# Kernel optimization log

Hardware: AMD Instinct MI355X
Metric: run time of the kernel (lower is better)

## Reference

```python
import jax, jax.numpy as jnp
import numpy as np

H, KVH, D, EPS = 8, 4, 64, 1e-5

def _rmsnorm(x, w):
    # normalize over last dim (head_dim)
    norm = jax.lax.rsqrt(jnp.mean(x * x, axis=-1, keepdims=True) + EPS)
    return x * norm * w

def setup_inputs() -> dict:
    key = jax.random.key(0)
    ks = jax.random.split(key, 5)
    B, S, Hid = 2048, 67, 512
    x = jax.random.normal(ks[0], (B, S, Hid), dtype=jnp.float32)
    # weights stored as [in, out] (equivalent to torch Linear weight.T)
    sc = 1.0 / np.sqrt(Hid)
    wq = jax.random.normal(ks[1], (Hid, H * D), dtype=jnp.float32) * sc
    wk = jax.random.normal(ks[2], (Hid, KVH * D), dtype=jnp.float32) * sc
    wv = jax.random.normal(ks[3], (Hid, KVH * D), dtype=jnp.float32) * sc
    wo = jax.random.normal(ks[4], (H * D, Hid), dtype=jnp.float32) * sc
    q_norm_w = jnp.ones((D,), dtype=jnp.float32)
    k_norm_w = jnp.ones((D,), dtype=jnp.float32)
    return {"x": x, "wq": wq, "wk": wk, "wv": wv, "wo": wo,
            "q_norm_w": q_norm_w, "k_norm_w": k_norm_w}

def reference(x, wq, wk, wv, wo, q_norm_w, k_norm_w):
    B, S, _ = x.shape
    G = H // KVH  # query heads per kv head
    q = (x @ wq).reshape(B, S, H, D).transpose(0, 2, 1, 3)      # (B,H,S,D)
    k = (x @ wk).reshape(B, S, KVH, D).transpose(0, 2, 1, 3)    # (B,KVH,S,D)
    v = (x @ wv).reshape(B, S, KVH, D).transpose(0, 2, 1, 3)
    q = _rmsnorm(q, q_norm_w)
    k = _rmsnorm(k, k_norm_w)
    qg = q.reshape(B, KVH, G, S, D)
    scale = 1.0 / np.sqrt(D)
    # bidirectional GQA attention, no mask
    scores = jnp.einsum('bkgsd,bktd->bkgst', qg, k) * scale      # (B,KVH,G,S,S)
    attn = jax.nn.softmax(scores, axis=-1)
    out = jnp.einsum('bkgst,bktd->bkgsd', attn, v)               # (B,KVH,G,S,D)
    out = out.reshape(B, H, S, D).transpose(0, 2, 1, 3).reshape(B, S, H * D)
    return out @ wo
```

## Files before the change

### kernel.cpp

```cpp
#include <hip/hip_runtime.h>
#include <hip/hip_bf16.h>

typedef __attribute__((ext_vector_type(8))) short short8;
typedef __attribute__((ext_vector_type(4))) float f32x4;

#define B_   2048
#define S_   67
#define M_   (B_*S_)
#define HID_ 512
#define H_   8
#define KVH_ 4
#define D_   64

__device__ __forceinline__ unsigned f2bf_u(float f){
  union { __hip_bfloat16 h; unsigned short u; } c; c.h = __float2bfloat16(f); return (unsigned)c.u;
}
__device__ __forceinline__ float bfu2f(unsigned u){
  union { unsigned short u; __hip_bfloat16 h; } c; c.u = (unsigned short)u; return __bfloat162float(c.h);
}
__device__ __forceinline__ unsigned pack2(float a, float b){ return f2bf_u(a) | (f2bf_u(b) << 16); }

__device__ __forceinline__ void unpack8(uint4 v, float* o){
  o[0]=bfu2f(v.x & 0xffffu); o[1]=bfu2f(v.x >> 16);
  o[2]=bfu2f(v.y & 0xffffu); o[3]=bfu2f(v.y >> 16);
  o[4]=bfu2f(v.z & 0xffffu); o[5]=bfu2f(v.z >> 16);
  o[6]=bfu2f(v.w & 0xffffu); o[7]=bfu2f(v.w >> 16);
}

union S8 { short8 v; unsigned short u[8]; };

__global__ __launch_bounds__(256) void cvt_bf16(const float* __restrict__ src,
                                                unsigned short* __restrict__ dst){
  long i = (long)blockIdx.x*256 + threadIdx.x;
  const float4 a = reinterpret_cast<const float4*>(src)[2*i];
  const float4 b = reinterpret_cast<const float4*>(src)[2*i+1];
  uint4 u = { pack2(a.x,a.y), pack2(a.z,a.w), pack2(b.x,b.y), pack2(b.z,b.w) };
  reinterpret_cast<uint4*>(dst)[i] = u;
}

__global__ __launch_bounds__(256) void transpose_w(const float* __restrict__ src, int ncols,
                                                   unsigned short* __restrict__ dst, int row0){
  __shared__ float tile[32][33];
  const int tx = threadIdx.x & 31, ty = threadIdx.x >> 5;
  const int nb = blockIdx.x * 32, kb = blockIdx.y * 32;
  #pragma unroll
  for (int i = 0; i < 4; ++i){
    int r = ty + i*8;
    tile[r][tx] = src[(size_t)(kb + r)*ncols + nb + tx];
  }
  __syncthreads();
  #pragma unroll
  for (int i = 0; i < 4; ++i){
    int r = ty + i*8;
    dst[(size_t)(row0 + nb + r)*512 + kb + tx] = (unsigned short)f2bf_u(tile[tx][r]);
  }
}

template<bool OUT_F32>
__global__ __launch_bounds__(512, 2) void gemm3_k(const unsigned short* __restrict__ A,
                                                  const unsigned short* __restrict__ Bw,
                                                  void* __restrict__ outp, int nbx){
  __shared__ unsigned short Sh[2][2][256*64];

  const int Nld = nbx << 8;
  const int per = gridDim.x >> 3;
  const int wg  = (blockIdx.x & 7) * per + (blockIdx.x >> 3);
  const int m0 = (wg / nbx) * 256;
  const int n0 = (wg % nbx) * 256;

  const int t = threadIdx.x;
  const int l = t & 63;
  const int w = t >> 6;
  const int wr = w >> 2, wc = w & 3;
  const int lr = l & 15, lk = l >> 4;

  const int srow  = w*32 + (l >> 3);
  const int skblk = (l & 7) ^ (l >> 3);
  const unsigned short* Ag = A  + (size_t)(m0 + srow)*512 + skblk*8;
  const unsigned short* Bg = Bw + (size_t)(n0 + srow)*512 + skblk*8;

  f32x4 acc[8][4];
  #pragma unroll
  for (int f = 0; f < 8; ++f)
    #pragma unroll
    for (int g = 0; g < 4; ++g) acc[f][g] = (f32x4){0.f, 0.f, 0.f, 0.f};

#define STAGE_(tt) do{ \
    unsigned short* As_ = &Sh[(tt)&1][0][0]; \
    unsigned short* Bs_ = &Sh[(tt)&1][1][0]; \
    _Pragma("unroll") \
    for (int j = 0; j < 4; ++j){ \
      __builtin_amdgcn_global_load_lds((const unsigned int*)(Ag + (size_t)(j*8)*512 + (tt)*64), \
                                       (unsigned int*)(As_ + (w*32 + j*8)*64), 16, 0, 0); \
      __builtin_amdgcn_global_load_lds((const unsigned int*)(Bg + (size_t)(j*8)*512 + (tt)*64), \
                                       (unsigned int*)(Bs_ + (w*32 + j*8)*64), 16, 0, 0); \
    } }while(0)

  STAGE_(0);
  #pragma unroll
  for (int tt = 0; tt < 8; ++tt){
    if (tt < 7) STAGE_(tt + 1);
    if (tt < 7) asm volatile("s_waitcnt vmcnt(8)" ::: "memory");
    else        asm volatile("s_waitcnt vmcnt(0)" ::: "memory");
    __builtin_amdgcn_s_barrier();
    __builtin_amdgcn_sched_barrier(0);

    const unsigned short* As = &Sh[tt&1][0][0];
    const unsigned short* Bs = &Sh[tt&1][1][0];
    #pragma unroll
    for (int ks = 0; ks < 2; ++ks){
      const int pk = ((ks*4 + lk) ^ (l & 7)) * 8;
      short8 av[8], bv[4];
      #pragma unroll
      for (int f = 0; f < 8; ++f)
        av[f] = *reinterpret_cast<const short8*>(As + (wr*128 + f*16 + lr)*64 + pk);
      #pragma unroll
      for (int g = 0; g < 4; ++g)
        bv[g] = *reinterpret_cast<const short8*>(Bs + (wc*64 + g*16 + lr)*64 + pk);
      #pragma unroll
      for (int f = 0; f < 8; ++f)
        #pragma unroll
        for (int g = 0; g < 4; ++g)
          acc[f][g] = __builtin_amdgcn_mfma_f32_16x16x32_bf16(av[f], bv[g], acc[f][g], 0, 0, 0);
    }
    asm volatile("s_waitcnt lgkmcnt(0)" ::: "memory");
    __builtin_amdgcn_sched_barrier(0);
    __builtin_amdgcn_s_barrier();
  }
#undef STAGE_

  if (OUT_F32){
    float* out = (float*)outp;
    #pragma unroll
    for (int f = 0; f < 8; ++f)
      #pragma unroll
      for (int g = 0; g < 4; ++g)
        #pragma unroll
        for (int r = 0; r < 4; ++r){
          size_t row = (size_t)(m0 + wr*128 + f*16 + lk*4 + r);
          out[row*Nld + n0 + wc*64 + g*16 + lr] = acc[f][g][r];
        }
  } else {
    unsigned short* Cs = &Sh[0][0][0];
    unsigned short* out = (unsigned short*)outp;
    #pragma unroll
    for (int half = 0; half < 2; ++half){
      __syncthreads();
      if (wr == half){
        #pragma unroll
        for (int f = 0; f < 8; ++f)
          #pragma unroll
          for (int g = 0; g < 4; ++g)
            #pragma unroll
            for (int r = 0; r < 4; ++r){
              int row = f*16 + lk*4 + r;
              int col = wc*64 + g*16 + lr;
              Cs[row*256 + col] = (unsigned short)f2bf_u(acc[f][g][r]);
            }
      }
      __syncthreads();
      const uint4* Cv = reinterpret_cast<const uint4*>(Cs);
      #pragma unroll
      for (int p = 0; p < 8; ++p){
        int idx = p*512 + t;
        int row = idx >> 5, c16 = idx & 31;
        *reinterpret_cast<uint4*>(out + (size_t)(m0 + half*128 + row)*Nld + n0 + c16*8) = Cv[idx];
      }
    }
  }
}

__global__ __launch_bounds__(576, 5) void attn_k(const unsigned short* __restrict__ qkv,
                                                 const float* __restrict__ qnw,
                                                 const float* __restrict__ knw,
                                                 unsigned short* __restrict__ attn){
  __shared__ unsigned short Vt[64*128];
  __shared__ unsigned short Kf[5][2][64*8];
  __shared__ unsigned short Pb[9][16*128];
  const int t = threadIdx.x;
  const int b = blockIdx.x >> 2, kvh = blockIdx.x & 3;
  const size_t rowbase = (size_t)b * 67;
  const int l = t & 63, w = t >> 6;
  const int lr = l & 15, lk = l >> 4;

  const int vs = t >> 3, vd0 = (t & 7) << 3;
  uint4 vu = {0u,0u,0u,0u};
  if (vs < 67)
    vu = *reinterpret_cast<const uint4*>(qkv + (rowbase + vs)*1024 + 768 + kvh*64 + vd0);
  uint4 ku0 = {0u,0u,0u,0u}, ku1 = {0u,0u,0u,0u};
  if (w < 5){
    int s = w*16 + lr; if (s > 66) s = 66;
    const unsigned short* kp = qkv + (rowbase + s)*1024 + 512 + kvh*64 + lk*8;
    ku0 = *reinterpret_cast<const uint4*>(kp);
    ku1 = *reinterpret_cast<const uint4*>(kp + 32);
  }
  const int qrow = w*16 + lr;
  const int h01 = (qrow >= 67) ? 1 : 0;
  int qr = qrow - (h01 ? 67 : 0); if (qr > 66) qr = 66;
  const unsigned short* qp = qkv + (rowbase + qr)*1024 + (kvh*2 + h01)*64 + lk*8;
  const uint4 qu0 = *reinterpret_cast<const uint4*>(qp);
  const uint4 qu1 = *reinterpret_cast<const uint4*>(qp + 32);
  float wp[16];
  #pragma unroll
  for (int hh = 0; hh < 2; ++hh)
    #pragma unroll
    for (int j = 0; j < 8; ++j){
      int idx = hh*32 + lk*8 + j;
      wp[hh*8+j] = qnw[idx] * knw[idx] * 0.125f;
    }

  {
    unsigned short vsv[8];
    vsv[0]=vu.x&0xffffu; vsv[1]=vu.x>>16; vsv[2]=vu.y&0xffffu; vsv[3]=vu.y>>16;
    vsv[4]=vu.z&0xffffu; vsv[5]=vu.z>>16; vsv[6]=vu.w&0xffffu; vsv[7]=vu.w>>16;
    #pragma unroll
    for (int j = 0; j < 8; ++j){
      int d = vd0 + j;
      int blk = ((vs>>3) ^ (j<<1) ^ (t&7)) & 15;
      Vt[(d<<7) + (blk<<3) + (vs&7)] = vsv[j];
    }
    if (t < 192){
      int s2 = 72 + (t >> 3);
      #pragma unroll
      for (int j = 0; j < 8; ++j){
        int d = vd0 + j;
        int blk = ((s2>>3) ^ (j<<1) ^ (t&7)) & 15;
        Vt[(d<<7) + (blk<<3) + (s2&7)] = 0;
      }
    }
  }

  if (w < 5){
    float f[16]; unpack8(ku0, f); unpack8(ku1, f + 8);
    float ss = 0.f;
    #pragma unroll
    for (int j = 0; j < 16; ++j) ss += f[j]*f[j];
    ss += __shfl_xor(ss, 16); ss += __shfl_xor(ss, 32);
    float inv = rsqrtf(ss*(1.0f/64.0f) + 1e-5f);
    S8 a0, a1;
    #pragma unroll
    for (int j = 0; j < 8; ++j){
      a0.u[j] = (unsigned short)f2bf_u(f[j]   * inv * wp[j]);
      a1.u[j] = (unsigned short)f2bf_u(f[8+j] * inv * wp[8+j]);
    }
    *reinterpret_cast<short8*>(&Kf[w][0][l*8]) = a0.v;
    *reinterpret_cast<short8*>(&Kf[w][1][l*8]) = a1.v;
  }

  short8 qf0, qf1;
  {
    float f[16]; unpack8(qu0, f); unpack8(qu1, f + 8);
    float ss = 0.f;
    #pragma unroll
    for (int j = 0; j < 16; ++j) ss += f[j]*f[j];
    ss += __shfl_xor(ss, 16); ss += __shfl_xor(ss, 32);
    float inv = rsqrtf(ss*(1.0f/64.0f) + 1e-5f);
    S8 a0, a1;
    #pragma unroll
    for (int j = 0; j < 8; ++j){
      a0.u[j] = (unsigned short)f2bf_u(f[j]   * inv);
      a1.u[j] = (unsigned short)f2bf_u(f[8+j] * inv);
    }
    qf0 = a0.v; qf1 = a1.v;
  }

  {
    uint4 z = {0u,0u,0u,0u};
    uint4* pz = reinterpret_cast<uint4*>(Pb[w]);
    #pragma unroll
    for (int i = 0; i < 4; ++i) pz[l + i*64] = z;
  }
  __syncthreads();

  f32x4 sa[5];
  #pragma unroll
  for (int nt = 0; nt < 5; ++nt){
    short8 k0 = *reinterpret_cast<const short8*>(&Kf[nt][0][l*8]);
    short8 k1 = *reinterpret_cast<const short8*>(&Kf[nt][1][l*8]);
    sa[nt] = (f32x4){0.f,0.f,0.f,0.f};
    sa[nt] = __builtin_amdgcn_mfma_f32_16x16x32_bf16(qf0, k0, sa[nt], 0,0,0);
    sa[nt] = __builtin_amdgcn_mfma_f32_16x16x32_bf16(qf1, k1, sa[nt], 0,0,0);
  }

  float inv4[4];
  #pragma unroll
  for (int r = 0; r < 4; ++r){
    float mx = -1e30f;
    #pragma unroll
    for (int nt = 0; nt < 5; ++nt){
      float v = sa[nt][r];
      if (nt*16 + lr >= 67) v = -1e30f;
      sa[nt][r] = v; mx = fmaxf(mx, v);
    }
    mx = fmaxf(mx, __shfl_xor(mx, 1));
    mx = fmaxf(mx, __shfl_xor(mx, 2));
    mx = fmaxf(mx, __shfl_xor(mx, 4));
    mx = fmaxf(mx, __shfl_xor(mx, 8));
    float sm = 0.f;
    #pragma unroll
    for (int nt = 0; nt < 5; ++nt){
      float e = __expf(sa[nt][r] - mx);
      sa[nt][r] = e; sm += e;
    }
    sm += __shfl_xor(sm, 1);
    sm += __shfl_xor(sm, 2);
    sm += __shfl_xor(sm, 4);
    sm += __shfl_xor(sm, 8);
    inv4[r] = 1.0f / sm;
  }

  unsigned short* pb = Pb[w];
  #pragma unroll
  for (int nt = 0; nt < 5; ++nt)
    #pragma unroll
    for (int r = 0; r < 4; ++r){
      int row = lk*4 + r, col = nt*16 + lr;
      int blk = ((col>>3) ^ ((row&7)<<1) ^ (row>>3)) & 15;
      pb[(row<<7) + (blk<<3) + (col&7)] = (unsigned short)f2bf_u(sa[nt][r]);
    }

  f32x4 oa[4];
  #pragma unroll
  for (int dt = 0; dt < 4; ++dt) oa[dt] = (f32x4){0.f,0.f,0.f,0.f};
  #pragma unroll
  for (int ks = 0; ks < 3; ++ks){
    int blkp = ((ks*4 + lk) ^ ((lr&7)<<1) ^ (lr>>3)) & 15;
    short8 pf = *reinterpret_cast<const short8*>(&pb[(lr<<7) + (blkp<<3)]);
    #pragma unroll
    for (int dt = 0; dt < 4; ++dt){
      int d = dt*16 + lr;
      int blkv = ((ks*4 + lk) ^ ((d&7)<<1) ^ (d>>3)) & 15;
      short8 vf = *reinterpret_cast<const short8*>(&Vt[(d<<7) + (blkv<<3)]);
      oa[dt] = __builtin_amdgcn_mfma_f32_16x16x32_bf16(pf, vf, oa[dt], 0,0,0);
    }
  }

  #pragma unroll
  for (int dt = 0; dt < 4; ++dt)
    #pragma unroll
    for (int r = 0; r < 4; ++r){
      int row = w*16 + lk*4 + r;
      if (row < 134){
        int hh = (row >= 67) ? 1 : 0;
        int orow = row - (hh ? 67 : 0);
        attn[(rowbase + orow)*512 + (kvh*2 + hh)*64 + dt*16 + lr] =
            (unsigned short)f2bf_u(oa[dt][r] * inv4[r]);
      }
    }
}

extern "C" void kernel_launch(void* const* d_in, const int* in_sizes, int n_in,
                              void* d_out, int out_size, void* d_ws, size_t ws_size,
                              hipStream_t stream){
  const float* x   = (const float*)d_in[0];
  const float* wq  = (const float*)d_in[1];
  const float* wk  = (const float*)d_in[2];
  const float* wv  = (const float*)d_in[3];
  const float* wo  = (const float*)d_in[4];
  const float* qnw = (const float*)d_in[5];
  const float* knw = (const float*)d_in[6];

  unsigned short* Wt   = (unsigned short*)d_ws;
  unsigned short* Wot  = Wt + 1024*512;
  unsigned short* qkv  = Wot + 512*512;
  unsigned short* attn = qkv + (size_t)M_*1024;
  unsigned short* xb   = attn;

  transpose_w<<<dim3(16,16), 256, 0, stream>>>(wq, 512, Wt, 0);
  transpose_w<<<dim3(8,16),  256, 0, stream>>>(wk, 256, Wt, 512);
  transpose_w<<<dim3(8,16),  256, 0, stream>>>(wv, 256, Wt, 768);
  transpose_w<<<dim3(16,16), 256, 0, stream>>>(wo, 512, Wot, 0);

  cvt_bf16<<<(M_*512/8 + 255)/256, 256, 0, stream>>>(x, xb);

  gemm3_k<false><<<dim3(4 * (M_/256)), 512, 0, stream>>>(xb, Wt, qkv, 4);

  attn_k<<<dim3(B_*KVH_), 576, 0, stream>>>(qkv, qnw, knw, attn);

  gemm3_k<true><<<dim3(2 * (M_/256)), 512, 0, stream>>>(attn, Wot, d_out, 2);
}
```

Before: 598.9 us.

## Fuse fp32-to-bf16 input conversion into QKV GEMM and coalesce fp32 output stores

Drops the separate cvt_bf16 pass. The QKV GEMM now loads fp32 x rows into registers, converts them to bf16 and writes them into swizzled LDS. A new wait and barrier schedule overlaps this with the async B-tile loads. The output projection now stages its fp32 results through LDS so each row is written with coalesced float4 stores instead of scattered scalar stores, and s_setprio is raised around the MFMA block. The fused load reads fp32 x four times, once per N-tile block, instead of bf16 once, so global traffic for A rises while a full round trip of the x conversion goes away.

```diff
diff --git a/kernel.cpp b/kernel.cpp
--- a/kernel.cpp
+++ b/kernel.cpp
@@ -29,15 +29,6 @@
 
 union S8 { short8 v; unsigned short u[8]; };
 
-__global__ __launch_bounds__(256) void cvt_bf16(const float* __restrict__ src,
-                                                unsigned short* __restrict__ dst){
-  long i = (long)blockIdx.x*256 + threadIdx.x;
-  const float4 a = reinterpret_cast<const float4*>(src)[2*i];
-  const float4 b = reinterpret_cast<const float4*>(src)[2*i+1];
-  uint4 u = { pack2(a.x,a.y), pack2(a.z,a.w), pack2(b.x,b.y), pack2(b.z,b.w) };
-  reinterpret_cast<uint4*>(dst)[i] = u;
-}
-
 __global__ __launch_bounds__(256) void transpose_w(const float* __restrict__ src, int ncols,
                                                    unsigned short* __restrict__ dst, int row0){
   __shared__ float tile[32][33];
@@ -56,8 +47,8 @@
   }
 }
 
-template<bool OUT_F32>
-__global__ __launch_bounds__(512, 2) void gemm3_k(const unsigned short* __restrict__ A,
+template<bool A_F32, bool OUT_F32>
+__global__ __launch_bounds__(512, 2) void gemm3_k(const void* __restrict__ Ap,
                                                   const unsigned short* __restrict__ Bw,
                                                   void* __restrict__ outp, int nbx){
   __shared__ unsigned short Sh[2][2][256*64];
@@ -76,34 +67,71 @@
 
   const int srow  = w*32 + (l >> 3);
   const int skblk = (l & 7) ^ (l >> 3);
-  const unsigned short* Ag = A  + (size_t)(m0 + srow)*512 + skblk*8;
+  const unsigned short* Ag = nullptr;
+  if (!A_F32) Ag = (const unsigned short*)Ap + (size_t)(m0 + srow)*512 + skblk*8;
   const unsigned short* Bg = Bw + (size_t)(n0 + srow)*512 + skblk*8;
 
+  const int arow_l = t >> 1, akh = t & 1;
+  const float4* xr = nullptr;
+  if (A_F32) xr = (const float4*)((const float*)Ap + (size_t)(m0 + arow_l)*512) + akh*8;
+  float4 vA[8];
+
   f32x4 acc[8][4];
   #pragma unroll
   for (int f = 0; f < 8; ++f)
     #pragma unroll
     for (int g = 0; g < 4; ++g) acc[f][g] = (f32x4){0.f, 0.f, 0.f, 0.f};
 
-#define STAGE_(tt) do{ \
-    unsigned short* As_ = &Sh[(tt)&1][0][0]; \
+#define STAGE_B_(tt) do{ \
     unsigned short* Bs_ = &Sh[(tt)&1][1][0]; \
     _Pragma("unroll") \
-    for (int j = 0; j < 4; ++j){ \
+    for (int j = 0; j < 4; ++j) \
+      __builtin_amdgcn_global_load_lds((const unsigned int*)(Bg + (size_t)(j*8)*512 + (tt)*64), \
+                                       (unsigned int*)(Bs_ + (w*32 + j*8)*64), 16, 0, 0); \
+  }while(0)
+#define STAGE_A_(tt) do{ \
+    unsigned short* As_ = &Sh[(tt)&1][0][0]; \
+    _Pragma("unroll") \
+    for (int j = 0; j < 4; ++j) \
       __builtin_amdgcn_global_load_lds((const unsigned int*)(Ag + (size_t)(j*8)*512 + (tt)*64), \
                                        (unsigned int*)(As_ + (w*32 + j*8)*64), 16, 0, 0); \
-      __builtin_amdgcn_global_load_lds((const unsigned int*)(Bg + (size_t)(j*8)*512 + (tt)*64), \
-                                       (unsigned int*)(Bs_ + (w*32 + j*8)*64), 16, 0, 0); \
+  }while(0)
+#define LOAD_VA_(tt) do{ \
+    _Pragma("unroll") \
+    for (int jj = 0; jj < 8; ++jj) vA[jj] = xr[(tt)*16 + jj]; \
+  }while(0)
+#define WRITE_VA_(tt) do{ \
+    unsigned short* As_ = &Sh[(tt)&1][0][0]; \
+    _Pragma("unroll") \
+    for (int j = 0; j < 4; ++j){ \
+      float4 a = vA[2*j], b = vA[2*j+1]; \
+      uint4 u = { pack2(a.x,a.y), pack2(a.z,a.w), pack2(b.x,b.y), pack2(b.z,b.w) }; \
+      int phys = (akh*4 + j) ^ (arow_l & 7); \
+      *reinterpret_cast<uint4*>(As_ + arow_l*64 + phys*8) = u; \
     } }while(0)
 
-  STAGE_(0);
+  if (A_F32){ LOAD_VA_(0); STAGE_B_(0); }
+  else      { STAGE_A_(0); STAGE_B_(0); }
+
   #pragma unroll
   for (int tt = 0; tt < 8; ++tt){
-    if (tt < 7) STAGE_(tt + 1);
-    if (tt < 7) asm volatile("s_waitcnt vmcnt(8)" ::: "memory");
-    else        asm volatile("s_waitcnt vmcnt(0)" ::: "memory");
-    __builtin_amdgcn_s_barrier();
-    __builtin_amdgcn_sched_barrier(0);
+    if (A_F32){
+      asm volatile("s_waitcnt vmcnt(4)" ::: "memory");
+      __builtin_amdgcn_sched_barrier(0);
+      WRITE_VA_(tt);
+      if (tt < 7){ LOAD_VA_(tt + 1); STAGE_B_(tt + 1); }
+      if (tt < 7) asm volatile("s_waitcnt vmcnt(12)" ::: "memory");
+      else        asm volatile("s_waitcnt vmcnt(0)"  ::: "memory");
+      asm volatile("s_waitcnt lgkmcnt(0)" ::: "memory");
+      __builtin_amdgcn_sched_barrier(0);
+      __builtin_amdgcn_s_barrier();
+    } else {
+      if (tt < 7){ STAGE_A_(tt + 1); STAGE_B_(tt + 1); }
+      if (tt < 7) asm volatile("s_waitcnt vmcnt(8)" ::: "memory");
+      else        asm volatile("s_waitcnt vmcnt(0)" ::: "memory");
+      __builtin_amdgcn_s_barrier();
+      __builtin_amdgcn_sched_barrier(0);
+    }
 
     const unsigned short* As = &Sh[tt&1][0][0];
     const unsigned short* Bs = &Sh[tt&1][1][0];
@@ -117,29 +145,50 @@
       #pragma unroll
       for (int g = 0; g < 4; ++g)
         bv[g] = *reinterpret_cast<const short8*>(Bs + (wc*64 + g*16 + lr)*64 + pk);
+      __builtin_amdgcn_s_setprio(1);
       #pragma unroll
       for (int f = 0; f < 8; ++f)
         #pragma unroll
         for (int g = 0; g < 4; ++g)
           acc[f][g] = __builtin_amdgcn_mfma_f32_16x16x32_bf16(av[f], bv[g], acc[f][g], 0, 0, 0);
+      __builtin_amdgcn_s_setprio(0);
     }
     asm volatile("s_waitcnt lgkmcnt(0)" ::: "memory");
     __builtin_amdgcn_sched_barrier(0);
     __builtin_amdgcn_s_barrier();
   }
-#undef STAGE_
+#undef STAGE_B_
+#undef STAGE_A_
+#undef LOAD_VA_
+#undef WRITE_VA_
 
   if (OUT_F32){
+    float* Cs = reinterpret_cast<float*>(&Sh[0][0][0]);
     float* out = (float*)outp;
     #pragma unroll
-    for (int f = 0; f < 8; ++f)
-      #pragma unroll
-      for (int g = 0; g < 4; ++g)
+    for (int half = 0; half < 2; ++half){
+      __syncthreads();
+      if (wr == half){
         #pragma unroll
-        for (int r = 0; r < 4; ++r){
-          size_t row = (size_t)(m0 + wr*128 + f*16 + lk*4 + r);
-          out[row*Nld + n0 + wc*64 + g*16 + lr] = acc[f][g][r];
-        }
+        for (int f = 0; f < 8; ++f)
+          #pragma unroll
+          for (int g = 0; g < 4; ++g)
+            #pragma unroll
+            for (int r = 0; r < 4; ++r){
+              int row = f*16 + lk*4 + r;
+              int col = wc*64 + g*16 + lr;
+              Cs[row*256 + col] = acc[f][g][r];
+            }
+      }
+      __syncthreads();
+      const float4* Cv = reinterpret_cast<const float4*>(Cs);
+      #pragma unroll
+      for (int p = 0; p < 16; ++p){
+        int idx = p*512 + t;
+        int row = idx >> 6, c4 = idx & 63;
+        *reinterpret_cast<float4*>(out + (size_t)(m0 + half*128 + row)*Nld + n0 + c4*4) = Cv[idx];
+      }
+    }
   } else {
     unsigned short* Cs = &Sh[0][0][0];
     unsigned short* out = (unsigned short*)outp;
@@ -364,18 +413,15 @@
   unsigned short* Wot  = Wt + 1024*512;
   unsigned short* qkv  = Wot + 512*512;
   unsigned short* attn = qkv + (size_t)M_*1024;
-  unsigned short* xb   = attn;
 
   transpose_w<<<dim3(16,16), 256, 0, stream>>>(wq, 512, Wt, 0);
   transpose_w<<<dim3(8,16),  256, 0, stream>>>(wk, 256, Wt, 512);
   transpose_w<<<dim3(8,16),  256, 0, stream>>>(wv, 256, Wt, 768);
   transpose_w<<<dim3(16,16), 256, 0, stream>>>(wo, 512, Wot, 0);
 
-  cvt_bf16<<<(M_*512/8 + 255)/256, 256, 0, stream>>>(x, xb);
-
-  gemm3_k<false><<<dim3(4 * (M_/256)), 512, 0, stream>>>(xb, Wt, qkv, 4);
+  gemm3_k<true, false><<<dim3(4 * (M_/256)), 512, 0, stream>>>(x, Wt, qkv, 4);
 
   attn_k<<<dim3(B_*KVH_), 576, 0, stream>>>(qkv, qnw, knw, attn);
 
-  gemm3_k<true><<<dim3(2 * (M_/256)), 512, 0, stream>>>(attn, Wot, d_out, 2);
-}
+  gemm3_k<false, true><<<dim3(2 * (M_/256)), 512, 0, stream>>>(attn, Wot, d_out, 2);
+}
```

Measured after the change: 683.6 us. +14.1%, slower.

## Restructure GEMM into 4-stage K=32 pipeline with interleaved loads and staged F32 epilogue

Applied to the files above, without the earlier changes.

The GEMM main loop now uses a four-deep ring of LDS buffers holding 32-wide K slices instead of a double buffer of 64-wide slices. Global-to-LDS loads for the slice two steps ahead are issued per operand inside each half-phase, with finer vmcnt waits, s_setprio around the MFMA bursts, and a new XOR swizzle for the narrower rows. The F32 output epilogue now stages results through LDS and writes coalesced float4 rows instead of scattered scalar stores. This aims to overlap memory with MFMA work and improve store efficiency, at the cost of more barriers and more complex synchronization.

```diff
diff --git a/kernel.cpp b/kernel.cpp
--- a/kernel.cpp
+++ b/kernel.cpp
@@ -57,10 +57,10 @@
 }
 
 template<bool OUT_F32>
-__global__ __launch_bounds__(512, 2) void gemm3_k(const unsigned short* __restrict__ A,
+__global__ __launch_bounds__(512, 2) void gemm5_k(const unsigned short* __restrict__ A,
                                                   const unsigned short* __restrict__ Bw,
                                                   void* __restrict__ outp, int nbx){
-  __shared__ unsigned short Sh[2][2][256*64];
+  __shared__ unsigned short Sh[4][2][256*32];
 
   const int Nld = nbx << 8;
   const int per = gridDim.x >> 3;
@@ -74,10 +74,12 @@
   const int wr = w >> 2, wc = w & 3;
   const int lr = l & 15, lk = l >> 4;
 
-  const int srow  = w*32 + (l >> 3);
-  const int skblk = (l & 7) ^ (l >> 3);
-  const unsigned short* Ag = A  + (size_t)(m0 + srow)*512 + skblk*8;
-  const unsigned short* Bg = Bw + (size_t)(n0 + srow)*512 + skblk*8;
+  const int srow  = w*16 + (l >> 2);
+  const int skblk = (l & 3) ^ ((l >> 2) & 3) ^ ((l >> 4) & 3);
+  const unsigned short* Ag0 = A  + (size_t)(m0 + srow)*512 + skblk*8;
+  const unsigned short* Bg0 = Bw + (size_t)(n0 + srow)*512 + skblk*8;
+
+  const int pk = (lk ^ (lr & 3) ^ ((lr >> 2) & 3)) * 8;
 
   f32x4 acc[8][4];
   #pragma unroll
@@ -85,61 +87,87 @@
     #pragma unroll
     for (int g = 0; g < 4; ++g) acc[f][g] = (f32x4){0.f, 0.f, 0.f, 0.f};
 
-#define STAGE_(tt) do{ \
-    unsigned short* As_ = &Sh[(tt)&1][0][0]; \
-    unsigned short* Bs_ = &Sh[(tt)&1][1][0]; \
+  short8 bv[4];
+
+#define STAGE_OP_(op_, kt_) do{ \
+    const unsigned short* src_ = ((op_) ? Bg0 : Ag0) + (size_t)(kt_)*32; \
+    unsigned short* dst_ = &Sh[(kt_)&3][op_][(w*16)*32]; \
+    __builtin_amdgcn_global_load_lds((const unsigned int*)src_, (unsigned int*)dst_, 16, 0, 0); \
+    __builtin_amdgcn_global_load_lds((const unsigned int*)(src_ + (size_t)128*512), \
+                                     (unsigned int*)(dst_ + 128*32), 16, 0, 0); \
+  }while(0)
+
+#define PHASE_(kt_, q_) do{ \
+    const unsigned short* Asl = &Sh[(kt_)&3][0][0]; \
+    const unsigned short* Bsl = &Sh[(kt_)&3][1][0]; \
+    short8 av[4]; \
     _Pragma("unroll") \
-    for (int j = 0; j < 4; ++j){ \
-      __builtin_amdgcn_global_load_lds((const unsigned int*)(Ag + (size_t)(j*8)*512 + (tt)*64), \
-                                       (unsigned int*)(As_ + (w*32 + j*8)*64), 16, 0, 0); \
-      __builtin_amdgcn_global_load_lds((const unsigned int*)(Bg + (size_t)(j*8)*512 + (tt)*64), \
-                                       (unsigned int*)(Bs_ + (w*32 + j*8)*64), 16, 0, 0); \
-    } }while(0)
-
-  STAGE_(0);
-  #pragma unroll
-  for (int tt = 0; tt < 8; ++tt){
-    if (tt < 7) STAGE_(tt + 1);
-    if (tt < 7) asm volatile("s_waitcnt vmcnt(8)" ::: "memory");
-    else        asm volatile("s_waitcnt vmcnt(0)" ::: "memory");
-    __builtin_amdgcn_s_barrier();
-    __builtin_amdgcn_sched_barrier(0);
-
-    const unsigned short* As = &Sh[tt&1][0][0];
-    const unsigned short* Bs = &Sh[tt&1][1][0];
-    #pragma unroll
-    for (int ks = 0; ks < 2; ++ks){
-      const int pk = ((ks*4 + lk) ^ (l & 7)) * 8;
-      short8 av[8], bv[4];
+    for (int f2 = 0; f2 < 4; ++f2) \
+      av[f2] = *reinterpret_cast<const short8*>(Asl + (wr*128 + ((q_)*4 + f2)*16 + lr)*32 + pk); \
+    if ((q_) == 0){ \
+      _Pragma("unroll") \
+      for (int g = 0; g < 4; ++g) \
+        bv[g] = *reinterpret_cast<const short8*>(Bsl + (wc*64 + g*16 + lr)*32 + pk); \
+    } \
+    if ((kt_) + 2 <= 15) STAGE_OP_((q_), (kt_) + 2); \
+    __builtin_amdgcn_s_barrier(); \
+    asm volatile("s_waitcnt lgkmcnt(0)" ::: "memory"); \
+    __builtin_amdgcn_sched_barrier(0); \
+    __builtin_amdgcn_s_setprio(1); \
+    _Pragma("unroll") \
+    for (int f2 = 0; f2 < 4; ++f2) \
+      _Pragma("unroll") \
+      for (int g = 0; g < 4; ++g) \
+        acc[(q_)*4 + f2][g] = __builtin_amdgcn_mfma_f32_16x16x32_bf16(av[f2], bv[g], acc[(q_)*4 + f2][g], 0, 0, 0); \
+    __builtin_amdgcn_s_setprio(0); \
+    if ((q_) == 1){ \
+      if ((kt_) < 14)       { asm volatile("s_waitcnt vmcnt(4)" ::: "memory"); } \
+      else if ((kt_) == 14) { asm volatile("s_waitcnt vmcnt(0)" ::: "memory"); } \
+      __builtin_amdgcn_sched_barrier(0); \
+    } \
+    __builtin_amdgcn_s_barrier(); \
+  }while(0)
+
+  STAGE_OP_(0, 0); STAGE_OP_(1, 0); STAGE_OP_(0, 1); STAGE_OP_(1, 1);
+  asm volatile("s_waitcnt vmcnt(4)" ::: "memory");
+  __builtin_amdgcn_sched_barrier(0);
+  __builtin_amdgcn_s_barrier();
+
+  #pragma unroll
+  for (int kt = 0; kt < 16; ++kt){
+    PHASE_(kt, 0);
+    PHASE_(kt, 1);
+  }
+#undef PHASE_
+#undef STAGE_OP_
+
+  if (OUT_F32){
+    float* Cs = reinterpret_cast<float*>(&Sh[0][0][0]);
+    float* out = (float*)outp;
+    #pragma unroll
+    for (int half = 0; half < 2; ++half){
+      __syncthreads();
+      if (wr == half){
+        #pragma unroll
+        for (int f = 0; f < 8; ++f)
+          #pragma unroll
+          for (int g = 0; g < 4; ++g)
+            #pragma unroll
+            for (int r = 0; r < 4; ++r){
+              int row = f*16 + lk*4 + r;
+              int col = wc*64 + g*16 + lr;
+              Cs[row*256 + col] = acc[f][g][r];
+            }
+      }
+      __syncthreads();
+      const float4* Cv = reinterpret_cast<const float4*>(Cs);
       #pragma unroll
-      for (int f = 0; f < 8; ++f)
-        av[f] = *reinterpret_cast<const short8*>(As + (wr*128 + f*16 + lr)*64 + pk);
-      #pragma unroll
-      for (int g = 0; g < 4; ++g)
-        bv[g] = *reinterpret_cast<const short8*>(Bs + (wc*64 + g*16 + lr)*64 + pk);
-      #pragma unroll
-      for (int f = 0; f < 8; ++f)
-        #pragma unroll
-        for (int g = 0; g < 4; ++g)
-          acc[f][g] = __builtin_amdgcn_mfma_f32_16x16x32_bf16(av[f], bv[g], acc[f][g], 0, 0, 0);
-    }
-    asm volatile("s_waitcnt lgkmcnt(0)" ::: "memory");
-    __builtin_amdgcn_sched_barrier(0);
-    __builtin_amdgcn_s_barrier();
-  }
-#undef STAGE_
-
-  if (OUT_F32){
-    float* out = (float*)outp;
-    #pragma unroll
-    for (int f = 0; f < 8; ++f)
-      #pragma unroll
-      for (int g = 0; g < 4; ++g)
-        #pragma unroll
-        for (int r = 0; r < 4; ++r){
-          size_t row = (size_t)(m0 + wr*128 + f*16 + lk*4 + r);
-          out[row*Nld + n0 + wc*64 + g*16 + lr] = acc[f][g][r];
-        }
+      for (int p = 0; p < 16; ++p){
+        int idx = p*512 + t;
+        int row = idx >> 6, c4 = idx & 63;
+        *reinterpret_cast<float4*>(out + (size_t)(m0 + half*128 + row)*Nld + n0 + c4*4) = Cv[idx];
+      }
+    }
   } else {
     unsigned short* Cs = &Sh[0][0][0];
     unsigned short* out = (unsigned short*)outp;
@@ -371,11 +399,11 @@
   transpose_w<<<dim3(8,16),  256, 0, stream>>>(wv, 256, Wt, 768);
   transpose_w<<<dim3(16,16), 256, 0, stream>>>(wo, 512, Wot, 0);
 
-  cvt_bf16<<<(M_*512/8 + 255)/256, 256, 0, stream>>>(x, xb);
-
-  gemm3_k<false><<<dim3(4 * (M_/256)), 512, 0, stream>>>(xb, Wt, qkv, 4);
+  cvt_bf16<<<(M_*512/8)/256, 256, 0, stream>>>(x, xb);
+
+  gemm5_k<false><<<dim3(4 * (M_/256)), 512, 0, stream>>>(xb, Wt, qkv, 4);
 
   attn_k<<<dim3(B_*KVH_), 576, 0, stream>>>(qkv, qnw, knw, attn);
 
-  gemm3_k<true><<<dim3(2 * (M_/256)), 512, 0, stream>>>(attn, Wot, d_out, 2);
-}
+  gemm5_k<true><<<dim3(2 * (M_/256)), 512, 0, stream>>>(attn, Wot, d_out, 2);
+}
```

Measured after the change: 580.9 us. 3.0% less time.
